# Kernel optimization log

Measured on AMD Instinct MI355X. Metric: run time of the kernel, lower is better.

## Reference

```python
import jax, jax.numpy as jnp
import numpy as np

EPS = 1e-5
NHEAD = 8

def layer_norm(x, g, b):
    mu = jnp.mean(x, axis=-1, keepdims=True)
    var = jnp.mean((x - mu) ** 2, axis=-1, keepdims=True)
    return (x - mu) * jax.lax.rsqrt(var + EPS) * g + b

def setup_inputs() -> dict:
    key = jax.random.key(0)
    ks = jax.random.split(key, 8)
    B, S, D, F = 4, 2048, 512, 2048
    s = 0.02
    return {
        "x": jax.random.normal(ks[0], (B, S, D), jnp.float32),
        "Wqkv": jax.random.normal(ks[1], (3 * D, D), jnp.float32) * s,
        "bqkv": jnp.zeros((3 * D,), jnp.float32),
        "Wo": jax.random.normal(ks[2], (D, D), jnp.float32) * s,
        "bo": jnp.zeros((D,), jnp.float32),
        "W1": jax.random.normal(ks[3], (F, D), jnp.float32) * s,
        "b1": jnp.zeros((F,), jnp.float32),
        "W2": jax.random.normal(ks[4], (D, F), jnp.float32) * s,
        "b2": jnp.zeros((D,), jnp.float32),
        "g1": jnp.ones((D,), jnp.float32),
        "bn1": jnp.zeros((D,), jnp.float32),
        "g2": jnp.ones((D,), jnp.float32),
        "bn2": jnp.zeros((D,), jnp.float32),
    }

def reference(x, Wqkv, bqkv, Wo, bo, W1, b1, W2, b2, g1, bn1, g2, bn2):
    B, S, D = x.shape
    H = NHEAD
    hd = D // H
    # fused QKV projection (torch MultiheadAttention in_proj)
    qkv = x @ Wqkv.T + bqkv                      # [B,S,3D]
    q, k, v = jnp.split(qkv, 3, axis=-1)
    q = q.reshape(B, S, H, hd).transpose(0, 2, 1, 3)  # [B,H,S,hd]
    k = k.reshape(B, S, H, hd).transpose(0, 2, 1, 3)
    v = v.reshape(B, S, H, hd).transpose(0, 2, 1, 3)
    scores = jnp.einsum("bhqd,bhkd->bhqk", q, k) / jnp.sqrt(jnp.float32(hd))
    causal = jnp.tril(jnp.ones((S, S), bool))
    scores = jnp.where(causal, scores, jnp.float32(-jnp.inf))
    attn = jax.nn.softmax(scores, axis=-1)
    ctx = jnp.einsum("bhqk,bhkd->bhqd", attn, v)        # [B,H,S,hd]
    ctx = ctx.transpose(0, 2, 1, 3).reshape(B, S, D)
    attn_out = ctx @ Wo.T + bo
    # residual + LayerNorm 1
    x = layer_norm(x + attn_out, g1, bn1)
    # FFN (ReLU) + residual + LayerNorm 2
    ff = jax.nn.relu(x @ W1.T + b1) @ W2.T + b2
    x = layer_norm(x + ff, g2, bn2)
    return x
```

## Files before the change

### kernel.cpp

```cpp
#include <hip/hip_runtime.h>
#include <hip/hip_bf16.h>
#include <math.h>

#define D_MODEL 512
#define SEQ     2048
#define BATCH   4
#define NHEADS  8
#define HDIM    64
#define FFN     2048
#define TOKENS  (BATCH*SEQ)

typedef __attribute__((ext_vector_type(8))) short bf16x8;
typedef __attribute__((ext_vector_type(4))) float f32x4;

__device__ inline ushort f2bf(float f) {
    unsigned u = __builtin_bit_cast(unsigned, f);
    unsigned r = (u + 0x7fffu + ((u >> 16) & 1u)) >> 16;
    return (ushort)r;
}
__device__ inline ushort f2bf_fast(float f) {
    return (ushort)((__builtin_bit_cast(unsigned, f) + 0x8000u) >> 16);
}

#define GLOAD_LDS16(g, l) __builtin_amdgcn_global_load_lds( \
    (const __attribute__((address_space(1))) void*)(g), \
    (__attribute__((address_space(3))) void*)(l), 16, 0, 0)

__global__ void cast_all_bf16(const float* __restrict__ x, const float* __restrict__ Wqkv,
                              const float* __restrict__ Wo, const float* __restrict__ W1,
                              const float* __restrict__ W2, ushort* __restrict__ outbase) {
    const int i = blockIdx.x * blockDim.x + threadIdx.x;
    if (i >= 1835008) return;
    float4 v;
    if      (i < 1048576) v = ((const float4*)x)[i];
    else if (i < 1245184) v = ((const float4*)Wqkv)[i - 1048576];
    else if (i < 1310720) v = ((const float4*)Wo)[i - 1245184];
    else if (i < 1572864) v = ((const float4*)W1)[i - 1310720];
    else                  v = ((const float4*)W2)[i - 1572864];
    ushort4 o;
    o.x = f2bf(v.x); o.y = f2bf(v.y); o.z = f2bf(v.z); o.w = f2bf(v.w);
    ((ushort4*)outbase)[i] = o;
}

template<int MODE, int RELU>
__global__ __launch_bounds__(256) void gemm_bt_mfma(const ushort* __restrict__ A,
                                                    const ushort* __restrict__ W,
                                                    const float* __restrict__ bias,
                                                    void* __restrict__ CoutA,
                                                    void* __restrict__ CoutB,
                                                    ushort* __restrict__ Qc,
                                                    ushort* __restrict__ Kc,
                                                    ushort* __restrict__ Vt,
                                                    int M, int N, int Kstride, int Klen) {
    __shared__ ushort Asb[128 * 32];
    __shared__ ushort Bsb[128 * 32];

    const int tid  = threadIdx.x;
    const int lane = tid & 63;
    const int wv   = tid >> 6;
    const int m0   = blockIdx.y * 128;
    const int n0   = blockIdx.x * 128;
    const int wm   = (wv >> 1) * 64;
    const int wn   = (wv & 1) * 64;
    const int ksel = (MODE == 3) ? blockIdx.z : 0;

    const ushort* Ab = A + (size_t)ksel * Klen;
    const ushort* Wb = W + (size_t)ksel * Klen;

    const int eA = wv * 1024 + lane * 8;
    const int rA = eA >> 5, cA = eA & 31;
    const ushort* gA0 = Ab + (size_t)(m0 + rA) * Kstride + cA;
    const ushort* gA1 = gA0 + (size_t)16 * Kstride;
    const ushort* gB0 = Wb + (size_t)(n0 + rA) * Kstride + cA;
    const ushort* gB1 = gB0 + (size_t)16 * Kstride;
    ushort* lA0 = Asb + wv * 1024;
    ushort* lA1 = Asb + wv * 1024 + 512;
    ushort* lB0 = Bsb + wv * 1024;
    ushort* lB1 = Bsb + wv * 1024 + 512;

    f32x4 acc[4][4] = {};

    const int fr = lane & 15;
    const int fk = (lane >> 4) * 8;

    for (int k0 = 0; k0 < Klen; k0 += 32) {
        GLOAD_LDS16(gA0, lA0); GLOAD_LDS16(gA1, lA1);
        GLOAD_LDS16(gB0, lB0); GLOAD_LDS16(gB1, lB1);
        gA0 += 32; gA1 += 32; gB0 += 32; gB1 += 32;
        __syncthreads();

        bf16x8 af[4], bfr[4];
        #pragma unroll
        for (int i = 0; i < 4; ++i)
            af[i] = *(const bf16x8*)(Asb + (wm + i * 16 + fr) * 32 + fk);
        #pragma unroll
        for (int j = 0; j < 4; ++j)
            bfr[j] = *(const bf16x8*)(Bsb + (wn + j * 16 + fr) * 32 + fk);

        #pragma unroll
        for (int i = 0; i < 4; ++i)
            #pragma unroll
            for (int j = 0; j < 4; ++j)
                acc[i][j] = __builtin_amdgcn_mfma_f32_16x16x32_bf16(af[i], bfr[j], acc[i][j], 0, 0, 0);
        __syncthreads();
    }

    const int col  = lane & 15;
    const int rowq = (lane >> 4) * 4;
    #pragma unroll
    for (int i = 0; i < 4; ++i) {
        const int gm = m0 + wm + i * 16 + rowq;
        #pragma unroll
        for (int j = 0; j < 4; ++j) {
            const int gn = n0 + wn + j * 16 + col;
            if (MODE == 2) {
                const float bv = bias[gn];
                const int seg = gn >> 9;
                const int h   = (gn >> 6) & 7;
                const int dd  = gn & 63;
                const int bb  = gm >> 11;
                const int ss  = gm & 2047;
                const int bh  = bb * 8 + h;
                if (seg == 2) {
                    ushort4 pk;
                    pk.x = f2bf(acc[i][j][0] + bv);
                    pk.y = f2bf(acc[i][j][1] + bv);
                    pk.z = f2bf(acc[i][j][2] + bv);
                    pk.w = f2bf(acc[i][j][3] + bv);
                    *(ushort4*)(Vt + ((size_t)bh * 64 + dd) * 2048 + ss) = pk;
                } else {
                    ushort* dst = (seg == 0 ? Qc : Kc) + ((size_t)bh * 2048 + ss) * 64 + dd;
                    #pragma unroll
                    for (int r = 0; r < 4; ++r)
                        dst[(size_t)r * 64] = f2bf(acc[i][j][r] + bv);
                }
            } else if (MODE == 3) {
                float* dst = (float*)(ksel ? CoutB : CoutA);
                const float bv = ksel ? 0.f : bias[gn];
                #pragma unroll
                for (int r = 0; r < 4; ++r)
                    dst[(size_t)(gm + r) * N + gn] = acc[i][j][r] + bv;
            } else {
                const float bv = bias[gn];
                #pragma unroll
                for (int r = 0; r < 4; ++r) {
                    float v = acc[i][j][r] + bv;
                    if (RELU) v = fmaxf(v, 0.f);
                    ((ushort*)CoutA)[(size_t)(gm + r) * N + gn] = f2bf(v);
                }
            }
        }
    }
}

__device__ __forceinline__ void attn_step(const ushort* __restrict__ Kb,
                                          const ushort* __restrict__ Vb,
                                          ushort* __restrict__ Psw,
                                          bf16x8 qf0, bf16x8 qf1,
                                          float (&lp)[4], f32x4 (&o)[4],
                                          int qw, int j0, bool diag,
                                          int col, int g, int c7) {
    f32x4 s[4] = {};
    #pragma unroll
    for (int nt = 0; nt < 4; ++nt) {
        const int kr = nt * 16 + col;
        bf16x8 kf0 = *(const bf16x8*)(Kb + kr * 64 + (((g    ) ^ c7) * 8));
        bf16x8 kf1 = *(const bf16x8*)(Kb + kr * 64 + (((g + 4) ^ c7) * 8));
        s[nt] = __builtin_amdgcn_mfma_f32_16x16x32_bf16(qf0, kf0, s[nt], 0, 0, 0);
        s[nt] = __builtin_amdgcn_mfma_f32_16x16x32_bf16(qf1, kf1, s[nt], 0, 0, 0);
    }

    if (diag) {
        #pragma unroll
        for (int nt = 0; nt < 4; ++nt)
            #pragma unroll
            for (int r = 0; r < 4; ++r)
                if ((j0 + nt * 16 + col) > (qw + 4 * g + r)) s[nt][r] = -INFINITY;
    }

    #pragma unroll
    for (int nt = 0; nt < 4; ++nt)
        #pragma unroll
        for (int r = 0; r < 4; ++r) {
            float p = __expf(s[nt][r] * 0.125f);
            s[nt][r] = p;
            lp[r] += p;
        }

    #pragma unroll
    for (int nt = 0; nt < 4; ++nt)
        #pragma unroll
        for (int r = 0; r < 4; ++r) {
            const int q  = 4 * g + r;
            const int bc = 32 * nt + 2 * col;
            *(ushort*)((char*)Psw + q * 128 + (((bc >> 4) ^ (q & 7)) * 16) + (bc & 15)) =
                f2bf_fast(s[nt][r]);
        }

    {
        bf16x8 pf0 = *(const bf16x8*)(Psw + col * 64 + (((g    ) ^ c7) * 8));
        bf16x8 pf1 = *(const bf16x8*)(Psw + col * 64 + (((g + 4) ^ c7) * 8));
        #pragma unroll
        for (int nt = 0; nt < 4; ++nt) {
            const int vr = nt * 16 + col;
            bf16x8 vf0 = *(const bf16x8*)(Vb + vr * 64 + (((g    ) ^ c7) * 8));
            bf16x8 vf1 = *(const bf16x8*)(Vb + vr * 64 + (((g + 4) ^ c7) * 8));
            o[nt] = __builtin_amdgcn_mfma_f32_16x16x32_bf16(pf0, vf0, o[nt], 0, 0, 0);
            o[nt] = __builtin_amdgcn_mfma_f32_16x16x32_bf16(pf1, vf1, o[nt], 0, 0, 0);
        }
    }
}

__global__ __launch_bounds__(256) void attn_mfma_kernel(const ushort* __restrict__ Qc,
                                                        const ushort* __restrict__ Kc,
                                                        const ushort* __restrict__ Vt,
                                                        ushort* __restrict__ ctxb) {
    __shared__ ushort Ks[2 * 64 * 64];
    __shared__ ushort Vs[2 * 64 * 64];
    __shared__ ushort Ps[64 * 64];

    const int tid  = threadIdx.x;
    const int lane = tid & 63;
    const int wv   = tid >> 6;
    const int pair = blockIdx.x;
    const int bh   = blockIdx.y;
    const int q0a  = pair * 64;
    const int q0b  = (31 - pair) * 64;
    const int qwA  = q0a + wv * 16;
    const int qwB  = q0b + wv * 16;

    const int col = lane & 15;
    const int g   = lane >> 4;
    const int c7  = col & 7;

    bf16x8 qfA0, qfA1, qfB0, qfB1;
    {
        const ushort* qa = Qc + ((size_t)bh * 2048 + qwA + col) * 64 + g * 8;
        qfA0 = *(const bf16x8*)qa;
        qfA1 = *(const bf16x8*)(qa + 32);
        const ushort* qb = Qc + ((size_t)bh * 2048 + qwB + col) * 64 + g * 8;
        qfB0 = *(const bf16x8*)qb;
        qfB1 = *(const bf16x8*)(qb + 32);
    }

    const int srow = tid >> 2;
    const int sch  = 2 * (tid & 3);
    const ushort* Kg = Kc + ((size_t)bh * 2048 + srow) * 64 + sch * 8;
    const ushort* Vg = Vt + ((size_t)bh * 64 + srow) * 2048 + sch * 8;
    const int ko0 = srow * 64 + (((sch    ) ^ (srow & 7)) * 8);
    const int ko1 = srow * 64 + (((sch + 1) ^ (srow & 7)) * 8);
    ushort* Psw = Ps + wv * 1024;

    float lpa[4] = {}, lpb[4] = {};
    f32x4 oa[4] = {}, ob[4] = {};

    bf16x8 pk0 = *(const bf16x8*)(Kg);
    bf16x8 pk1 = *(const bf16x8*)(Kg + 8);
    bf16x8 pv0 = *(const bf16x8*)(Vg);
    bf16x8 pv1 = *(const bf16x8*)(Vg + 8);

    for (int j0 = 0; j0 <= q0b; j0 += 64) {
        const int par = (j0 >> 6) & 1;
        ushort* Kb = Ks + par * 4096;
        ushort* Vb = Vs + par * 4096;
        *(bf16x8*)(Kb + ko0) = pk0; *(bf16x8*)(Kb + ko1) = pk1;
        *(bf16x8*)(Vb + ko0) = pv0; *(bf16x8*)(Vb + ko1) = pv1;
        __syncthreads();

        if (j0 < q0b) {
            pk0 = *(const bf16x8*)(Kg + (size_t)(j0 + 64) * 64);
            pk1 = *(const bf16x8*)(Kg + (size_t)(j0 + 64) * 64 + 8);
            pv0 = *(const bf16x8*)(Vg + j0 + 64);
            pv1 = *(const bf16x8*)(Vg + j0 + 72);
        }

        if (j0 <= q0a)
            attn_step(Kb, Vb, Psw, qfA0, qfA1, lpa, oa, qwA, j0, j0 == q0a, col, g, c7);
        attn_step(Kb, Vb, Psw, qfB0, qfB1, lpb, ob, qwB, j0, j0 == q0b, col, g, c7);
    }

    const int b = bh >> 3, h = bh & 7;
    #pragma unroll
    for (int r = 0; r < 4; ++r) {
        float la = lpa[r];
        la += __shfl_xor(la, 1); la += __shfl_xor(la, 2);
        la += __shfl_xor(la, 4); la += __shfl_xor(la, 8);
        float lb = lpb[r];
        lb += __shfl_xor(lb, 1); lb += __shfl_xor(lb, 2);
        lb += __shfl_xor(lb, 4); lb += __shfl_xor(lb, 8);
        const float inva = 1.f / la;
        const float invb = 1.f / lb;
        const size_t rowa = ((size_t)b * 2048 + qwA + 4 * g + r) * 512 + h * 64;
        const size_t rowb = ((size_t)b * 2048 + qwB + 4 * g + r) * 512 + h * 64;
        #pragma unroll
        for (int nt = 0; nt < 4; ++nt) {
            ctxb[rowa + nt * 16 + col] = f2bf(oa[nt][r] * inva);
            ctxb[rowb + nt * 16 + col] = f2bf(ob[nt][r] * invb);
        }
    }
}

template<int WRITE_BF16>
__global__ void ln_residual(const float* __restrict__ A, const float* __restrict__ B1,
                            const float* __restrict__ B2,
                            const float* __restrict__ g, const float* __restrict__ beta,
                            float* __restrict__ out, ushort* __restrict__ outb) {
    __shared__ float sbuf[8];
    const int row = blockIdx.x;
    const int tid = threadIdx.x;
    const size_t base = (size_t)row * D_MODEL;

    float v0 = A[base + tid]       + B1[base + tid]       + B2[base + tid];
    float v1 = A[base + tid + 256] + B1[base + tid + 256] + B2[base + tid + 256];

    float sum = v0 + v1;
    #pragma unroll
    for (int off = 32; off; off >>= 1) sum += __shfl_xor(sum, off);
    if ((tid & 63) == 0) sbuf[tid >> 6] = sum;
    __syncthreads();
    if (tid == 0) { float t = 0.f; for (int i = 0; i < 4; ++i) t += sbuf[i]; sbuf[4] = t; }
    __syncthreads();
    const float mu = sbuf[4] * (1.f / 512.f);
    __syncthreads();

    float d0 = v0 - mu, d1 = v1 - mu;
    float sq = d0 * d0 + d1 * d1;
    #pragma unroll
    for (int off = 32; off; off >>= 1) sq += __shfl_xor(sq, off);
    if ((tid & 63) == 0) sbuf[tid >> 6] = sq;
    __syncthreads();
    if (tid == 0) { float t = 0.f; for (int i = 0; i < 4; ++i) t += sbuf[i]; sbuf[4] = t; }
    __syncthreads();
    const float var = sbuf[4] * (1.f / 512.f);
    const float rs  = rsqrtf(var + 1e-5f);

    float r0 = d0 * rs * g[tid]       + beta[tid];
    float r1 = d1 * rs * g[tid + 256] + beta[tid + 256];
    out[base + tid]       = r0;
    out[base + tid + 256] = r1;
    if (WRITE_BF16) {
        outb[base + tid]       = f2bf(r0);
        outb[base + tid + 256] = f2bf(r1);
    }
}

extern "C" void kernel_launch(void* const* d_in, const int* in_sizes, int n_in,
                              void* d_out, int out_size, void* d_ws, size_t ws_size,
                              hipStream_t stream) {
    const float* x    = (const float*)d_in[0];
    const float* Wqkv = (const float*)d_in[1];
    const float* bqkv = (const float*)d_in[2];
    const float* Wo   = (const float*)d_in[3];
    const float* bo   = (const float*)d_in[4];
    const float* W1   = (const float*)d_in[5];
    const float* b1   = (const float*)d_in[6];
    const float* W2   = (const float*)d_in[7];
    const float* b2   = (const float*)d_in[8];
    const float* g1   = (const float*)d_in[9];
    const float* bn1  = (const float*)d_in[10];
    const float* g2   = (const float*)d_in[11];
    const float* bn2  = (const float*)d_in[12];

    float* ws = (float*)d_ws;
    ushort* Qcb     = (ushort*)ws;
    ushort* Kcb     = (ushort*)(ws + 2097152);
    ushort* Vtb     = (ushort*)(ws + 4194304);
    float*  attn_b  = ws;
    ushort* ff1b    = (ushort*)ws;
    float*  ff2a    = ws + 8388608;
    float*  attn_a  = ws + 12582912;
    float*  ff2b    = ws + 12582912;
    float*  ln1     = ws + 16777216;
    ushort* ctxb  = (ushort*)(ws + 20971520);
    ushort* ln1b  = (ushort*)(ws + 23068672);
    ushort* xb    = (ushort*)(ws + 25165824);
    ushort* Wqkvb = (ushort*)(ws + 27262976);
    float*  out   = (float*)d_out;
    ushort* W1b   = (ushort*)(ws + 27787264);
    ushort* W2b   = (ushort*)(ws + 28311552);
    ushort* Wob   = (ushort*)(ws + 27656192);

    const dim3 blk(256);

    cast_all_bf16<<<dim3(7168), blk, 0, stream>>>(x, Wqkv, Wo, W1, W2, xb);

    gemm_bt_mfma<2,0><<<dim3(1536/128, 8192/128), blk, 0, stream>>>(
        xb, Wqkvb, bqkv, nullptr, nullptr, Qcb, Kcb, Vtb, TOKENS, 1536, 512, 512);
    attn_mfma_kernel<<<dim3(16, BATCH*NHEADS), blk, 0, stream>>>(Qcb, Kcb, Vtb, ctxb);
    gemm_bt_mfma<3,0><<<dim3(512/128, 8192/128, 2), blk, 0, stream>>>(
        ctxb, Wob, bo, attn_a, attn_b, nullptr, nullptr, nullptr, TOKENS, 512, 512, 256);
    ln_residual<1><<<dim3(TOKENS), blk, 0, stream>>>(x, attn_a, attn_b, g1, bn1, ln1, ln1b);
    gemm_bt_mfma<1,1><<<dim3(2048/128, 8192/128), blk, 0, stream>>>(
        ln1b, W1b, b1, ff1b, nullptr, nullptr, nullptr, nullptr, TOKENS, 2048, 512, 512);
    gemm_bt_mfma<3,0><<<dim3(512/128, 8192/128, 2), blk, 0, stream>>>(
        ff1b, W2b, b2, ff2a, ff2b, nullptr, nullptr, nullptr, TOKENS, 512, 2048, 1024);
    ln_residual<0><<<dim3(TOKENS), blk, 0, stream>>>(ln1, ff2a, ff2b, g2, bn2, out, nullptr);
}
```

Baseline: 270.1 us.

## Store split-K partials in bf16, fuse residual into GEMM epilogue, double K-step

The split-K output projection and FFN2 GEMMs now write bf16 partials instead of fp32. The residual (x or the bf16 LN1 output) is folded into the first split's epilogue, so the layernorm kernels read only two bf16 buffers and no separate fp32 residual. LN1 no longer writes an fp32 copy, and the layernorms use vectorized loads and stores. The GEMM main loop now loads two 32-wide K slices per barrier pair, halving the synchronisations. The cost is extra bf16 rounding on the partials and on the residual path, which changes precision.

```diff
diff --git a/kernel.cpp b/kernel.cpp
--- a/kernel.cpp
+++ b/kernel.cpp
@@ -20,6 +20,9 @@
 }
 __device__ inline ushort f2bf_fast(float f) {
     return (ushort)((__builtin_bit_cast(unsigned, f) + 0x8000u) >> 16);
+}
+__device__ inline float bf2f(ushort u) {
+    return __builtin_bit_cast(float, (unsigned)u << 16);
 }
 
 #define GLOAD_LDS16(g, l) __builtin_amdgcn_global_load_lds( \
@@ -42,18 +45,19 @@
     ((ushort4*)outbase)[i] = o;
 }
 
-template<int MODE, int RELU>
+template<int MODE, int RELU, int RES>
 __global__ __launch_bounds__(256) void gemm_bt_mfma(const ushort* __restrict__ A,
                                                     const ushort* __restrict__ W,
                                                     const float* __restrict__ bias,
                                                     void* __restrict__ CoutA,
                                                     void* __restrict__ CoutB,
+                                                    const void* __restrict__ Res,
                                                     ushort* __restrict__ Qc,
                                                     ushort* __restrict__ Kc,
                                                     ushort* __restrict__ Vt,
                                                     int M, int N, int Kstride, int Klen) {
-    __shared__ ushort Asb[128 * 32];
-    __shared__ ushort Bsb[128 * 32];
+    __shared__ ushort Asb[2][128 * 32];
+    __shared__ ushort Bsb[2][128 * 32];
 
     const int tid  = threadIdx.x;
     const int lane = tid & 63;
@@ -73,35 +77,43 @@
     const ushort* gA1 = gA0 + (size_t)16 * Kstride;
     const ushort* gB0 = Wb + (size_t)(n0 + rA) * Kstride + cA;
     const ushort* gB1 = gB0 + (size_t)16 * Kstride;
-    ushort* lA0 = Asb + wv * 1024;
-    ushort* lA1 = Asb + wv * 1024 + 512;
-    ushort* lB0 = Bsb + wv * 1024;
-    ushort* lB1 = Bsb + wv * 1024 + 512;
+    ushort* lA0 = &Asb[0][wv * 1024];
+    ushort* lA1 = &Asb[0][wv * 1024 + 512];
+    ushort* lB0 = &Bsb[0][wv * 1024];
+    ushort* lB1 = &Bsb[0][wv * 1024 + 512];
+    ushort* lA0h = &Asb[1][wv * 1024];
+    ushort* lA1h = &Asb[1][wv * 1024 + 512];
+    ushort* lB0h = &Bsb[1][wv * 1024];
+    ushort* lB1h = &Bsb[1][wv * 1024 + 512];
 
     f32x4 acc[4][4] = {};
 
     const int fr = lane & 15;
     const int fk = (lane >> 4) * 8;
 
-    for (int k0 = 0; k0 < Klen; k0 += 32) {
-        GLOAD_LDS16(gA0, lA0); GLOAD_LDS16(gA1, lA1);
-        GLOAD_LDS16(gB0, lB0); GLOAD_LDS16(gB1, lB1);
-        gA0 += 32; gA1 += 32; gB0 += 32; gB1 += 32;
+    for (int k0 = 0; k0 < Klen; k0 += 64) {
+        GLOAD_LDS16(gA0, lA0);  GLOAD_LDS16(gA1, lA1);
+        GLOAD_LDS16(gB0, lB0);  GLOAD_LDS16(gB1, lB1);
+        GLOAD_LDS16(gA0 + 32, lA0h); GLOAD_LDS16(gA1 + 32, lA1h);
+        GLOAD_LDS16(gB0 + 32, lB0h); GLOAD_LDS16(gB1 + 32, lB1h);
+        gA0 += 64; gA1 += 64; gB0 += 64; gB1 += 64;
         __syncthreads();
 
-        bf16x8 af[4], bfr[4];
-        #pragma unroll
-        for (int i = 0; i < 4; ++i)
-            af[i] = *(const bf16x8*)(Asb + (wm + i * 16 + fr) * 32 + fk);
-        #pragma unroll
-        for (int j = 0; j < 4; ++j)
-            bfr[j] = *(const bf16x8*)(Bsb + (wn + j * 16 + fr) * 32 + fk);
-
-        #pragma unroll
-        for (int i = 0; i < 4; ++i)
+        #pragma unroll
+        for (int h = 0; h < 2; ++h) {
+            bf16x8 af[4], bfr[4];
+            #pragma unroll
+            for (int i = 0; i < 4; ++i)
+                af[i] = *(const bf16x8*)(&Asb[h][(wm + i * 16 + fr) * 32 + fk]);
             #pragma unroll
             for (int j = 0; j < 4; ++j)
-                acc[i][j] = __builtin_amdgcn_mfma_f32_16x16x32_bf16(af[i], bfr[j], acc[i][j], 0, 0, 0);
+                bfr[j] = *(const bf16x8*)(&Bsb[h][(wn + j * 16 + fr) * 32 + fk]);
+            #pragma unroll
+            for (int i = 0; i < 4; ++i)
+                #pragma unroll
+                for (int j = 0; j < 4; ++j)
+                    acc[i][j] = __builtin_amdgcn_mfma_f32_16x16x32_bf16(af[i], bfr[j], acc[i][j], 0, 0, 0);
+        }
         __syncthreads();
     }
 
@@ -135,11 +147,17 @@
                         dst[(size_t)r * 64] = f2bf(acc[i][j][r] + bv);
                 }
             } else if (MODE == 3) {
-                float* dst = (float*)(ksel ? CoutB : CoutA);
-                const float bv = ksel ? 0.f : bias[gn];
+                ushort* dst = (ushort*)(ksel ? CoutB : CoutA);
                 #pragma unroll
-                for (int r = 0; r < 4; ++r)
-                    dst[(size_t)(gm + r) * N + gn] = acc[i][j][r] + bv;
+                for (int r = 0; r < 4; ++r) {
+                    float v = acc[i][j][r];
+                    if (!ksel) {
+                        v += bias[gn];
+                        if (RES == 1) v += ((const float*)Res)[(size_t)(gm + r) * N + gn];
+                        if (RES == 2) v += bf2f(((const ushort*)Res)[(size_t)(gm + r) * N + gn]);
+                    }
+                    dst[(size_t)(gm + r) * N + gn] = f2bf(v);
+                }
             } else {
                 const float bv = bias[gn];
                 #pragma unroll
@@ -300,18 +318,19 @@
     }
 }
 
-template<int WRITE_BF16>
-__global__ void ln_residual(const float* __restrict__ A, const float* __restrict__ B1,
-                            const float* __restrict__ B2,
-                            const float* __restrict__ g, const float* __restrict__ beta,
-                            float* __restrict__ out, ushort* __restrict__ outb) {
+template<int OUTMODE>
+__global__ void ln_residual2(const ushort* __restrict__ B1, const ushort* __restrict__ B2,
+                             const float* __restrict__ g, const float* __restrict__ beta,
+                             float* __restrict__ out, ushort* __restrict__ outb) {
     __shared__ float sbuf[8];
     const int row = blockIdx.x;
     const int tid = threadIdx.x;
     const size_t base = (size_t)row * D_MODEL;
 
-    float v0 = A[base + tid]       + B1[base + tid]       + B2[base + tid];
-    float v1 = A[base + tid + 256] + B1[base + tid + 256] + B2[base + tid + 256];
+    ushort2 p1 = ((const ushort2*)(B1 + base))[tid];
+    ushort2 p2 = ((const ushort2*)(B2 + base))[tid];
+    float v0 = bf2f(p1.x) + bf2f(p2.x);
+    float v1 = bf2f(p1.y) + bf2f(p2.y);
 
     float sum = v0 + v1;
     #pragma unroll
@@ -334,13 +353,16 @@
     const float var = sbuf[4] * (1.f / 512.f);
     const float rs  = rsqrtf(var + 1e-5f);
 
-    float r0 = d0 * rs * g[tid]       + beta[tid];
-    float r1 = d1 * rs * g[tid + 256] + beta[tid + 256];
-    out[base + tid]       = r0;
-    out[base + tid + 256] = r1;
-    if (WRITE_BF16) {
-        outb[base + tid]       = f2bf(r0);
-        outb[base + tid + 256] = f2bf(r1);
+    float2 gv = ((const float2*)g)[tid];
+    float2 bv = ((const float2*)beta)[tid];
+    float r0 = d0 * rs * gv.x + bv.x;
+    float r1 = d1 * rs * gv.y + bv.y;
+    if (OUTMODE == 0) {
+        float2 o2; o2.x = r0; o2.y = r1;
+        ((float2*)(out + base))[tid] = o2;
+    } else {
+        ushort2 o2; o2.x = f2bf(r0); o2.y = f2bf(r1);
+        ((ushort2*)(outb + base))[tid] = o2;
     }
 }
 
@@ -362,37 +384,36 @@
     const float* bn2  = (const float*)d_in[12];
 
     float* ws = (float*)d_ws;
-    ushort* Qcb     = (ushort*)ws;
-    ushort* Kcb     = (ushort*)(ws + 2097152);
-    ushort* Vtb     = (ushort*)(ws + 4194304);
-    float*  attn_b  = ws;
-    ushort* ff1b    = (ushort*)ws;
-    float*  ff2a    = ws + 8388608;
-    float*  attn_a  = ws + 12582912;
-    float*  ff2b    = ws + 12582912;
-    float*  ln1     = ws + 16777216;
-    ushort* ctxb  = (ushort*)(ws + 20971520);
-    ushort* ln1b  = (ushort*)(ws + 23068672);
-    ushort* xb    = (ushort*)(ws + 25165824);
-    ushort* Wqkvb = (ushort*)(ws + 27262976);
-    float*  out   = (float*)d_out;
-    ushort* W1b   = (ushort*)(ws + 27787264);
-    ushort* W2b   = (ushort*)(ws + 28311552);
-    ushort* Wob   = (ushort*)(ws + 27656192);
+    ushort* Qcb    = (ushort*)ws;
+    ushort* Kcb    = (ushort*)(ws + 2097152);
+    ushort* Vtb    = (ushort*)(ws + 4194304);
+    ushort* ff1b   = (ushort*)ws;
+    ushort* attn_a = (ushort*)(ws + 8388608);
+    ushort* attn_b = (ushort*)(ws + 10485760);
+    ushort* ff2a   = (ushort*)(ws + 12582912);
+    ushort* ff2b   = (ushort*)(ws + 14680064);
+    ushort* ln1b   = (ushort*)(ws + 16777216);
+    ushort* ctxb   = (ushort*)(ws + 20971520);
+    ushort* xb     = (ushort*)(ws + 25165824);
+    ushort* Wqkvb  = (ushort*)(ws + 27262976);
+    ushort* Wob    = (ushort*)(ws + 27656192);
+    ushort* W1b    = (ushort*)(ws + 27787264);
+    ushort* W2b    = (ushort*)(ws + 28311552);
+    float*  out    = (float*)d_out;
 
     const dim3 blk(256);
 
     cast_all_bf16<<<dim3(7168), blk, 0, stream>>>(x, Wqkv, Wo, W1, W2, xb);
 
-    gemm_bt_mfma<2,0><<<dim3(1536/128, 8192/128), blk, 0, stream>>>(
-        xb, Wqkvb, bqkv, nullptr, nullptr, Qcb, Kcb, Vtb, TOKENS, 1536, 512, 512);
+    gemm_bt_mfma<2,0,0><<<dim3(12, 64), blk, 0, stream>>>(
+        xb, Wqkvb, bqkv, nullptr, nullptr, nullptr, Qcb, Kcb, Vtb, TOKENS, 1536, 512, 512);
     attn_mfma_kernel<<<dim3(16, BATCH*NHEADS), blk, 0, stream>>>(Qcb, Kcb, Vtb, ctxb);
-    gemm_bt_mfma<3,0><<<dim3(512/128, 8192/128, 2), blk, 0, stream>>>(
-        ctxb, Wob, bo, attn_a, attn_b, nullptr, nullptr, nullptr, TOKENS, 512, 512, 256);
-    ln_residual<1><<<dim3(TOKENS), blk, 0, stream>>>(x, attn_a, attn_b, g1, bn1, ln1, ln1b);
-    gemm_bt_mfma<1,1><<<dim3(2048/128, 8192/128), blk, 0, stream>>>(
-        ln1b, W1b, b1, ff1b, nullptr, nullptr, nullptr, nullptr, TOKENS, 2048, 512, 512);
-    gemm_bt_mfma<3,0><<<dim3(512/128, 8192/128, 2), blk, 0, stream>>>(
-        ff1b, W2b, b2, ff2a, ff2b, nullptr, nullptr, nullptr, TOKENS, 512, 2048, 1024);
-    ln_residual<0><<<dim3(TOKENS), blk, 0, stream>>>(ln1, ff2a, ff2b, g2, bn2, out, nullptr);
-}
+    gemm_bt_mfma<3,0,1><<<dim3(4, 64, 2), blk, 0, stream>>>(
+        ctxb, Wob, bo, attn_a, attn_b, x, nullptr, nullptr, nullptr, TOKENS, 512, 512, 256);
+    ln_residual2<1><<<dim3(TOKENS), blk, 0, stream>>>(attn_a, attn_b, g1, bn1, nullptr, ln1b);
+    gemm_bt_mfma<1,1,0><<<dim3(16, 64), blk, 0, stream>>>(
+        ln1b, W1b, b1, ff1b, nullptr, nullptr, nullptr, nullptr, nullptr, TOKENS, 2048, 512, 512);
+    gemm_bt_mfma<3,0,2><<<dim3(4, 64, 2), blk, 0, stream>>>(
+        ff1b, W2b, b2, ff2a, ff2b, ln1b, nullptr, nullptr, nullptr, TOKENS, 512, 2048, 1024);
+    ln_residual2<0><<<dim3(TOKENS), blk, 0, stream>>>(ff2a, ff2b, g2, bn2, out, nullptr);
+}
```

After: 271.6 us. Within noise of the previous version (+0.6%).
